# Kernel tuning notes

Measured on AMD Instinct MI355X. Metric: run time of the kernel, lower is better.

## Reference

```python
import jax, jax.numpy as jnp
import numpy as np

D_MODEL = 256
N_HEADS = 8
D_HEAD = D_MODEL // N_HEADS
SCALE = D_HEAD ** -0.5
LN_EPS = 1e-5


def _layernorm(x, gamma, beta):
    mu = jnp.mean(x, axis=-1, keepdims=True)
    var = jnp.mean(jnp.square(x - mu), axis=-1, keepdims=True)
    return (x - mu) * jax.lax.rsqrt(var + LN_EPS) * gamma + beta


def setup_inputs() -> dict:
    key = jax.random.key(0)
    ks = jax.random.split(key, 8)
    B, N_q, N_kv = 2, 1024, 8192
    q = jax.random.normal(ks[0], (B, N_q, D_MODEL), dtype=jnp.float32)
    kv = jax.random.normal(ks[1], (B, N_kv, D_MODEL), dtype=jnp.float32)
    attn_bias = jax.random.normal(ks[2], (B, N_HEADS, N_q, N_kv), dtype=jnp.float32)
    s = D_MODEL ** -0.5
    Wq = jax.random.normal(ks[3], (D_MODEL, D_MODEL), dtype=jnp.float32) * s
    Wk = jax.random.normal(ks[4], (D_MODEL, D_MODEL), dtype=jnp.float32) * s
    Wv = jax.random.normal(ks[5], (D_MODEL, D_MODEL), dtype=jnp.float32) * s
    Wo = jax.random.normal(ks[6], (D_MODEL, D_MODEL), dtype=jnp.float32) * s
    gamma_q = jnp.ones((D_MODEL,), jnp.float32)
    beta_q = jnp.zeros((D_MODEL,), jnp.float32)
    gamma_kv = jnp.ones((D_MODEL,), jnp.float32)
    beta_kv = jnp.zeros((D_MODEL,), jnp.float32)
    return dict(q=q, kv=kv, attn_bias=attn_bias, Wq=Wq, Wk=Wk, Wv=Wv, Wo=Wo,
                gamma_q=gamma_q, beta_q=beta_q, gamma_kv=gamma_kv, beta_kv=beta_kv)


def reference(q, kv, attn_bias, Wq, Wk, Wv, Wo, gamma_q, beta_q, gamma_kv, beta_kv):
    B, N_q, D = q.shape
    N_kv = kv.shape[1]
    q_n = _layernorm(q, gamma_q, beta_q)
    kv_n = _layernorm(kv, gamma_kv, beta_kv)
    # nn.Linear(x) = x @ W.T ; reshape to (B, H, N, dh)
    Q = (q_n @ Wq.T).reshape(B, N_q, N_HEADS, D_HEAD).transpose(0, 2, 1, 3)
    K = (kv_n @ Wk.T).reshape(B, N_kv, N_HEADS, D_HEAD).transpose(0, 2, 1, 3)
    V = (kv_n @ Wv.T).reshape(B, N_kv, N_HEADS, D_HEAD).transpose(0, 2, 1, 3)
    scores = jnp.einsum('bhqd,bhkd->bhqk', Q, K) * SCALE + attn_bias
    attn = jax.nn.softmax(scores, axis=-1)
    out = jnp.einsum('bhqk,bhkd->bhqd', attn, V)
    out = out.transpose(0, 2, 1, 3).reshape(B, N_q, D)
    return q + out @ Wo.T
```

## Files before the change

### kernel.cpp

```cpp
#include <hip/hip_runtime.h>
#include <hip/hip_bf16.h>
#include <stdint.h>

#define H 8
#define NQ 1024
#define NKV 8192
#define DM 256
#define DH 32
#define KVBLK 128
#define KSPLIT 8
#define NITER (NKV / KSPLIT / KVBLK)
#define SCALE 0.17677669529663687f

typedef __attribute__((ext_vector_type(8))) __bf16 bf16x8;
typedef __attribute__((ext_vector_type(4))) float f32x4;

__device__ inline unsigned short f2bf(float f) {
  unsigned int u = __builtin_bit_cast(unsigned int, f);
  u = (u + 0x7FFFu + ((u >> 16) & 1u)) >> 16;
  return (unsigned short)u;
}

__global__ void prep_kernel(const float* __restrict__ q, const float* __restrict__ kv,
                            const float* __restrict__ gq, const float* __restrict__ bq,
                            const float* __restrict__ gkv, const float* __restrict__ bkv,
                            const float* __restrict__ Wq, const float* __restrict__ Wk,
                            const float* __restrict__ Wv, const float* __restrict__ Wo,
                            unsigned short* __restrict__ qn, unsigned short* __restrict__ kvn,
                            unsigned short* __restrict__ Wqb, unsigned short* __restrict__ Wkb,
                            unsigned short* __restrict__ Wvb, unsigned short* __restrict__ Wob) {
  int bx = blockIdx.x;
  if (bx < 256) {
    int widx = bx >> 6, blk = bx & 63;
    const float* src; unsigned short* dst;
    if (widx == 0)      { src = Wq; dst = Wqb; }
    else if (widx == 1) { src = Wk; dst = Wkb; }
    else if (widx == 2) { src = Wv; dst = Wvb; }
    else                { src = Wo; dst = Wob; }
    int i = (blk * 256 + threadIdx.x) * 4;
    float4 v = *(const float4*)(src + i);
    unsigned int lo = (unsigned int)f2bf(v.x) | ((unsigned int)f2bf(v.y) << 16);
    unsigned int hi = (unsigned int)f2bf(v.z) | ((unsigned int)f2bf(v.w) << 16);
    *(uint2*)(dst + i) = make_uint2(lo, hi);
    return;
  }
  int row = (bx - 256) * 64 + (threadIdx.x >> 2);
  int l4 = threadIdx.x & 3;
  const float* src; const float* ga; const float* be; unsigned short* dst;
  if (row < 2048) {
    src = q + (long)row * DM; ga = gq; be = bq; dst = qn + (long)row * DM;
  } else {
    int r2 = row - 2048;
    src = kv + (long)r2 * DM; ga = gkv; be = bkv; dst = kvn + (long)r2 * DM;
  }
  int c0 = l4 * 64;
  float s = 0.f, ss = 0.f;
  float4 xv[16];
#pragma unroll
  for (int i = 0; i < 16; i++) {
    float4 v = *(const float4*)(src + c0 + i * 4);
    xv[i] = v;
    s += v.x + v.y + v.z + v.w;
    ss += v.x * v.x + v.y * v.y + v.z * v.z + v.w * v.w;
  }
  s += __shfl_xor(s, 1, 4);  s += __shfl_xor(s, 2, 4);
  ss += __shfl_xor(ss, 1, 4); ss += __shfl_xor(ss, 2, 4);
  float mean = s * (1.0f / 256.0f);
  float var = ss * (1.0f / 256.0f) - mean * mean;
  float rs = 1.0f / sqrtf(var + 1e-5f);
#pragma unroll
  for (int i = 0; i < 8; i++) {
    float4 a = xv[2 * i], b = xv[2 * i + 1];
    float4 g0 = *(const float4*)(ga + c0 + i * 8);
    float4 g1 = *(const float4*)(ga + c0 + i * 8 + 4);
    float4 b0 = *(const float4*)(be + c0 + i * 8);
    float4 b1 = *(const float4*)(be + c0 + i * 8 + 4);
    unsigned short t[8];
    t[0] = f2bf((a.x - mean) * rs * g0.x + b0.x);
    t[1] = f2bf((a.y - mean) * rs * g0.y + b0.y);
    t[2] = f2bf((a.z - mean) * rs * g0.z + b0.z);
    t[3] = f2bf((a.w - mean) * rs * g0.w + b0.w);
    t[4] = f2bf((b.x - mean) * rs * g1.x + b1.x);
    t[5] = f2bf((b.y - mean) * rs * g1.y + b1.y);
    t[6] = f2bf((b.z - mean) * rs * g1.z + b1.z);
    t[7] = f2bf((b.w - mean) * rs * g1.w + b1.w);
    unsigned int u0 = (unsigned int)t[0] | ((unsigned int)t[1] << 16);
    unsigned int u1 = (unsigned int)t[2] | ((unsigned int)t[3] << 16);
    unsigned int u2 = (unsigned int)t[4] | ((unsigned int)t[5] << 16);
    unsigned int u3 = (unsigned int)t[6] | ((unsigned int)t[7] << 16);
    *(uint4*)(dst + c0 + i * 8) = make_uint4(u0, u1, u2, u3);
  }
}

__global__ void proj_all_kernel(const unsigned short* __restrict__ qn, const unsigned short* __restrict__ kvn,
                                const unsigned short* __restrict__ Wqb, const unsigned short* __restrict__ Wkb,
                                const unsigned short* __restrict__ Wvb,
                                unsigned short* __restrict__ Qw, unsigned short* __restrict__ Kw,
                                unsigned short* __restrict__ Vtw) {
  int bx = blockIdx.x;
  const unsigned short* X; const unsigned short* Wb; unsigned short* out;
  int Nper, mode, mb;
  if (bx < 32)       { X = qn;  Wb = Wqb; out = Qw;  Nper = NQ;  mode = 0; mb = bx; }
  else if (bx < 288) { X = kvn; Wb = Wkb; out = Kw;  Nper = NKV; mode = 0; mb = bx - 32; }
  else               { X = kvn; Wb = Wvb; out = Vtw; Nper = NKV; mode = 1; mb = bx - 288; }

  int w = threadIdx.x >> 6, lane = threadIdx.x & 63;
  int c = lane & 15, g = lane >> 4;
  int mbase = mb * 64 + w * 16;
  f32x4 acc[16];
#pragma unroll
  for (int i = 0; i < 16; i++) acc[i] = (f32x4){0.f, 0.f, 0.f, 0.f};
  const unsigned short* arow = X + (long)(mbase + c) * DM + g * 8;
#pragma unroll
  for (int ks = 0; ks < 8; ks++) {
    bf16x8 af = *(const bf16x8*)(arow + ks * 32);
#pragma unroll
    for (int nt = 0; nt < 16; nt++) {
      bf16x8 bf = *(const bf16x8*)(Wb + (long)(nt * 16 + c) * DM + ks * 32 + g * 8);
      acc[nt] = __builtin_amdgcn_mfma_f32_16x16x32_bf16(af, bf, acc[nt], 0, 0, 0);
    }
  }
#pragma unroll
  for (int nt = 0; nt < 16; nt++) {
#pragma unroll
    for (int r = 0; r < 4; r++) {
      int m = mbase + 4 * g + r;
      int n = nt * 16 + c;
      int b = (m >= Nper) ? 1 : 0;
      int i = m - b * Nper;
      int h = n >> 5, dd = n & 31;
      long idx;
      if (mode == 0) idx = ((long)(b * H + h) * Nper + i) * DH + dd;
      else           idx = ((long)(b * H + h) * DH + dd) * (long)Nper + i;
      out[idx] = f2bf(acc[nt][r]);
    }
  }
}

__global__ __launch_bounds__(256, 4) void attn_kernel(
    const unsigned short* __restrict__ Qw, const unsigned short* __restrict__ Kw,
    const unsigned short* __restrict__ Vtw, const float* __restrict__ bias,
    float* __restrict__ Opart, float* __restrict__ Mpart, float* __restrict__ Lpart) {
  __shared__ __align__(16) unsigned short Klds[KVBLK * 40];
  __shared__ __align__(16) unsigned short Vlds[DH * 136];
  __shared__ __align__(16) unsigned short Plds[4][16 * 136];

  int bx = blockIdx.x;
  int s = bx & 7, qt = (bx >> 3) & 15, bh = bx >> 7;
  int tid = threadIdx.x;
  int w = tid >> 6, lane = tid & 63, c = lane & 15, g = lane >> 4;

  const f32x4 fzero = {0.f, 0.f, 0.f, 0.f};

  bf16x8 qfrag = *(const bf16x8*)(Qw + ((long)(bh * NQ + qt * 64 + w * 16 + c)) * DH + g * 8);

  const float* brow = bias + ((long)bh * NQ + qt * 64 + w * 16 + c) * (long)NKV + 4 * g;

  const unsigned short* Kbase = Kw + ((long)bh * NKV) * DH;
  const unsigned short* Vbase = Vtw + ((long)bh * DH) * NKV;

  float m_run = -1e30f;
  float l_run = 0.f;
  f32x4 oacc[2] = {fzero, fzero};

#pragma unroll 1
  for (int it = 0; it < NITER; it++) {
    int k0 = (it * KSPLIT + s) * KVBLK;

    f32x4 bfrag[8];
#pragma unroll
    for (int t = 0; t < 8; t++)
      bfrag[t] = *(const f32x4*)(brow + k0 + t * 16);

    {
      const unsigned short* src = Kbase + (long)k0 * DH;
#pragma unroll
      for (int rp = 0; rp < 2; rp++) {
        int row = (tid >> 2) + rp * 64;
        int q4 = tid & 3;
        *(uint4*)(&Klds[row * 40 + q4 * 8]) = *(const uint4*)(src + row * DH + q4 * 8);
      }
#pragma unroll
      for (int rp = 0; rp < 2; rp++) {
        int u = tid + rp * 256;
        int d = u >> 4, q16 = u & 15;
        *(uint4*)(&Vlds[d * 136 + q16 * 8]) = *(const uint4*)(Vbase + (long)d * NKV + k0 + q16 * 8);
      }
    }
    __syncthreads();

    f32x4 sacc[8];
#pragma unroll
    for (int t = 0; t < 8; t++) {
      bf16x8 kf = *(const bf16x8*)(&Klds[(t * 16 + c) * 40 + g * 8]);
      sacc[t] = __builtin_amdgcn_mfma_f32_16x16x32_bf16(kf, qfrag, fzero, 0, 0, 0);
    }
#pragma unroll
    for (int t = 0; t < 8; t++) {
#pragma unroll
      for (int r = 0; r < 4; r++)
        sacc[t][r] = fmaf(sacc[t][r], SCALE, bfrag[t][r]);
    }

    float v = -1e30f;
#pragma unroll
    for (int t = 0; t < 8; t++)
      v = fmaxf(v, fmaxf(fmaxf(sacc[t][0], sacc[t][1]), fmaxf(sacc[t][2], sacc[t][3])));
    v = fmaxf(v, __shfl_xor(v, 16));
    v = fmaxf(v, __shfl_xor(v, 32));
    float mnew = fmaxf(m_run, v);
    float al = __expf(m_run - mnew);
    m_run = mnew;
    float rsum = 0.f;
#pragma unroll
    for (int t = 0; t < 8; t++) {
      float p0 = __expf(sacc[t][0] - mnew);
      float p1 = __expf(sacc[t][1] - mnew);
      float p2 = __expf(sacc[t][2] - mnew);
      float p3 = __expf(sacc[t][3] - mnew);
      rsum += (p0 + p1) + (p2 + p3);
      uint2 pk;
      pk.x = (unsigned int)f2bf(p0) | ((unsigned int)f2bf(p1) << 16);
      pk.y = (unsigned int)f2bf(p2) | ((unsigned int)f2bf(p3) << 16);
      *(uint2*)(&Plds[w][c * 136 + t * 16 + 4 * g]) = pk;
    }
    rsum += __shfl_xor(rsum, 16);
    rsum += __shfl_xor(rsum, 32);
    l_run = l_run * al + rsum;

    float alq[4];
#pragma unroll
    for (int r = 0; r < 4; r++) alq[r] = __shfl(al, 4 * g + r);
#pragma unroll
    for (int r = 0; r < 4; r++) { oacc[0][r] *= alq[r]; oacc[1][r] *= alq[r]; }

#pragma unroll
    for (int ch = 0; ch < 4; ch++) {
      bf16x8 pf = *(const bf16x8*)(&Plds[w][c * 136 + ch * 32 + g * 8]);
#pragma unroll
      for (int dt = 0; dt < 2; dt++) {
        bf16x8 vf = *(const bf16x8*)(&Vlds[(dt * 16 + c) * 136 + ch * 32 + g * 8]);
        oacc[dt] = __builtin_amdgcn_mfma_f32_16x16x32_bf16(pf, vf, oacc[dt], 0, 0, 0);
      }
    }
    __syncthreads();
  }
  float* Op = Opart + (long)bx * (64 * 32);
#pragma unroll
  for (int dt = 0; dt < 2; dt++)
#pragma unroll
    for (int r = 0; r < 4; r++)
      Op[(w * 16 + 4 * g + r) * 32 + dt * 16 + c] = oacc[dt][r];
  if (g == 0) {
    Mpart[(long)bx * 64 + w * 16 + c] = m_run;
    Lpart[(long)bx * 64 + w * 16 + c] = l_run;
  }
}

__global__ void merge_outproj_kernel(const float* __restrict__ Opart, const float* __restrict__ Mpart,
                                     const float* __restrict__ Lpart, const unsigned short* __restrict__ Wob,
                                     const float* __restrict__ qin, float* __restrict__ out) {
  __shared__ __align__(16) unsigned short OmT[16][264];

  int bx = blockIdx.x;
  int b = bx >> 6, qt = (bx >> 2) & 15, q4 = bx & 3;
  int tid = threadIdx.x;

  int row16 = tid >> 4;
  int d0 = (tid & 15) * 2;
  int rowA = q4 * 16 + row16;
#pragma unroll 1
  for (int h = 0; h < 8; h++) {
    long pbase = ((long)(b * 8 + h) * 16 + qt) * 8;
    float mg = -1e30f, ms[8];
#pragma unroll
    for (int si = 0; si < 8; si++) {
      ms[si] = Mpart[(pbase + si) * 64 + rowA];
      mg = fmaxf(mg, ms[si]);
    }
    float Lg = 0.f;
    float o0 = 0.f, o1 = 0.f;
#pragma unroll
    for (int si = 0; si < 8; si++) {
      float wsc = __expf(ms[si] - mg);
      Lg += Lpart[(pbase + si) * 64 + rowA] * wsc;
      const float* op = Opart + (pbase + si) * 2048 + rowA * 32 + d0;
      o0 += op[0] * wsc;
      o1 += op[1] * wsc;
    }
    float inv = 1.0f / Lg;
    unsigned int u = (unsigned int)f2bf(o0 * inv) | ((unsigned int)f2bf(o1 * inv) << 16);
    *(unsigned int*)(&OmT[row16][h * 32 + d0]) = u;
  }
  __syncthreads();

  int w = tid >> 6, lane = tid & 63;
  int c = lane & 15, g = lane >> 4;
  long mglob = (long)b * NQ + qt * 64 + q4 * 16;
  f32x4 acc[4];
#pragma unroll
  for (int i = 0; i < 4; i++) acc[i] = (f32x4){0.f, 0.f, 0.f, 0.f};
#pragma unroll
  for (int ks = 0; ks < 8; ks++) {
    bf16x8 af = *(const bf16x8*)(&OmT[c][ks * 32 + g * 8]);
#pragma unroll
    for (int j = 0; j < 4; j++) {
      int nt = w * 4 + j;
      bf16x8 bf = *(const bf16x8*)(Wob + (long)(nt * 16 + c) * DM + ks * 32 + g * 8);
      acc[j] = __builtin_amdgcn_mfma_f32_16x16x32_bf16(af, bf, acc[j], 0, 0, 0);
    }
  }
#pragma unroll
  for (int j = 0; j < 4; j++) {
#pragma unroll
    for (int r = 0; r < 4; r++) {
      long m = mglob + 4 * g + r;
      int n = (w * 4 + j) * 16 + c;
      out[m * DM + n] = qin[m * DM + n] + acc[j][r];
    }
  }
}

extern "C" void kernel_launch(void* const* d_in, const int* in_sizes, int n_in,
                              void* d_out, int out_size, void* d_ws, size_t ws_size,
                              hipStream_t stream) {
  (void)in_sizes; (void)n_in; (void)out_size; (void)ws_size;
  const float* q    = (const float*)d_in[0];
  const float* kv   = (const float*)d_in[1];
  const float* bias = (const float*)d_in[2];
  const float* Wq   = (const float*)d_in[3];
  const float* Wk   = (const float*)d_in[4];
  const float* Wv   = (const float*)d_in[5];
  const float* Wo   = (const float*)d_in[6];
  const float* gq   = (const float*)d_in[7];
  const float* bq   = (const float*)d_in[8];
  const float* gkv  = (const float*)d_in[9];
  const float* bkv  = (const float*)d_in[10];
  float* out = (float*)d_out;

  char* ws = (char*)d_ws;
  size_t off = 0;
  auto alloc = [&](size_t bytes) -> void* {
    void* p = ws + off;
    off += (bytes + 255) & ~(size_t)255;
    return p;
  };
  unsigned short* Wqb  = (unsigned short*)alloc(65536 * 2);
  unsigned short* Wkb  = (unsigned short*)alloc(65536 * 2);
  unsigned short* Wvb  = (unsigned short*)alloc(65536 * 2);
  unsigned short* Wob  = (unsigned short*)alloc(65536 * 2);
  unsigned short* qn   = (unsigned short*)alloc((size_t)2048 * 256 * 2);
  unsigned short* kvn  = (unsigned short*)alloc((size_t)16384 * 256 * 2);
  unsigned short* Qw   = (unsigned short*)alloc((size_t)2048 * 256 * 2);
  unsigned short* Kw   = (unsigned short*)alloc((size_t)16384 * 256 * 2);
  unsigned short* Vtw  = (unsigned short*)alloc((size_t)16384 * 256 * 2);
  float* Opart = (float*)alloc((size_t)2048 * 2048 * 4);
  float* Mpart = (float*)alloc((size_t)2048 * 64 * 4);
  float* Lpart = (float*)alloc((size_t)2048 * 64 * 4);

  prep_kernel<<<544, 256, 0, stream>>>(q, kv, gq, bq, gkv, bkv, Wq, Wk, Wv, Wo,
                                       qn, kvn, Wqb, Wkb, Wvb, Wob);

  proj_all_kernel<<<544, 256, 0, stream>>>(qn, kvn, Wqb, Wkb, Wvb, Qw, Kw, Vtw);

  attn_kernel<<<2048, 256, 0, stream>>>(Qw, Kw, Vtw, bias, Opart, Mpart, Lpart);

  merge_outproj_kernel<<<128, 256, 0, stream>>>(Opart, Mpart, Lpart, Wob, q, out);
}
```

Before: 222.7 us.

## Fuse layernorm into projection GEMM and register-prefetch K/V and bias in attention

Splits weight conversion into its own small kernel and folds the layernorm of q/kv directly into the projection kernel. Normalized bf16 activations are now built in registers instead of going through a global round trip. The attention loop is restructured to prefetch the next K/V tile and the next bias fragments into registers while the current tile is computed. This hides global load latency at the cost of more registers and extra barriers. kv rows are now read and normalized twice, once each for the K and V projections.

```diff
diff --git a/kernel.cpp b/kernel.cpp
--- a/kernel.cpp
+++ b/kernel.cpp
@@ -21,99 +21,82 @@
   return (unsigned short)u;
 }
 
-__global__ void prep_kernel(const float* __restrict__ q, const float* __restrict__ kv,
-                            const float* __restrict__ gq, const float* __restrict__ bq,
-                            const float* __restrict__ gkv, const float* __restrict__ bkv,
-                            const float* __restrict__ Wq, const float* __restrict__ Wk,
-                            const float* __restrict__ Wv, const float* __restrict__ Wo,
-                            unsigned short* __restrict__ qn, unsigned short* __restrict__ kvn,
-                            unsigned short* __restrict__ Wqb, unsigned short* __restrict__ Wkb,
-                            unsigned short* __restrict__ Wvb, unsigned short* __restrict__ Wob) {
-  int bx = blockIdx.x;
-  if (bx < 256) {
-    int widx = bx >> 6, blk = bx & 63;
-    const float* src; unsigned short* dst;
-    if (widx == 0)      { src = Wq; dst = Wqb; }
-    else if (widx == 1) { src = Wk; dst = Wkb; }
-    else if (widx == 2) { src = Wv; dst = Wvb; }
-    else                { src = Wo; dst = Wob; }
-    int i = (blk * 256 + threadIdx.x) * 4;
-    float4 v = *(const float4*)(src + i);
+__global__ void wconv_kernel(const float* __restrict__ Wq, const float* __restrict__ Wk,
+                             const float* __restrict__ Wv, const float* __restrict__ Wo,
+                             unsigned short* __restrict__ Wqb, unsigned short* __restrict__ Wkb,
+                             unsigned short* __restrict__ Wvb, unsigned short* __restrict__ Wob) {
+  long i = ((long)blockIdx.x * 256 + threadIdx.x) * 16;
+  int widx = (int)(i >> 16);
+  int off = (int)(i & 65535);
+  const float* src; unsigned short* dst;
+  if (widx == 0)      { src = Wq; dst = Wqb; }
+  else if (widx == 1) { src = Wk; dst = Wkb; }
+  else if (widx == 2) { src = Wv; dst = Wvb; }
+  else                { src = Wo; dst = Wob; }
+#pragma unroll
+  for (int j = 0; j < 4; j++) {
+    float4 v = *(const float4*)(src + off + j * 4);
     unsigned int lo = (unsigned int)f2bf(v.x) | ((unsigned int)f2bf(v.y) << 16);
     unsigned int hi = (unsigned int)f2bf(v.z) | ((unsigned int)f2bf(v.w) << 16);
-    *(uint2*)(dst + i) = make_uint2(lo, hi);
-    return;
-  }
-  int row = (bx - 256) * 64 + (threadIdx.x >> 2);
-  int l4 = threadIdx.x & 3;
-  const float* src; const float* ga; const float* be; unsigned short* dst;
-  if (row < 2048) {
-    src = q + (long)row * DM; ga = gq; be = bq; dst = qn + (long)row * DM;
-  } else {
-    int r2 = row - 2048;
-    src = kv + (long)r2 * DM; ga = gkv; be = bkv; dst = kvn + (long)r2 * DM;
-  }
-  int c0 = l4 * 64;
+    *(uint2*)(dst + off + j * 4) = make_uint2(lo, hi);
+  }
+}
+
+__global__ void ln_proj_kernel(const float* __restrict__ qin, const float* __restrict__ kvin,
+                               const float* __restrict__ gq, const float* __restrict__ bq,
+                               const float* __restrict__ gkv, const float* __restrict__ bkv,
+                               const unsigned short* __restrict__ Wqb, const unsigned short* __restrict__ Wkb,
+                               const unsigned short* __restrict__ Wvb,
+                               unsigned short* __restrict__ Qw, unsigned short* __restrict__ Kw,
+                               unsigned short* __restrict__ Vtw) {
+  int bx = blockIdx.x;
+  const float* X; const float* ga; const float* be;
+  const unsigned short* Wb; unsigned short* out;
+  int Nper, mode, mb;
+  if (bx < 32)       { X = qin;  ga = gq;  be = bq;  Wb = Wqb; out = Qw;  Nper = NQ;  mode = 0; mb = bx; }
+  else if (bx < 288) { X = kvin; ga = gkv; be = bkv; Wb = Wkb; out = Kw;  Nper = NKV; mode = 0; mb = bx - 32; }
+  else               { X = kvin; ga = gkv; be = bkv; Wb = Wvb; out = Vtw; Nper = NKV; mode = 1; mb = bx - 288; }
+
+  int w = threadIdx.x >> 6, lane = threadIdx.x & 63;
+  int c = lane & 15, g = lane >> 4;
+  int mbase = mb * 64 + w * 16;
+  const float* xp = X + (long)(mbase + c) * DM + g * 8;
+
   float s = 0.f, ss = 0.f;
-  float4 xv[16];
-#pragma unroll
-  for (int i = 0; i < 16; i++) {
-    float4 v = *(const float4*)(src + c0 + i * 4);
-    xv[i] = v;
-    s += v.x + v.y + v.z + v.w;
-    ss += v.x * v.x + v.y * v.y + v.z * v.z + v.w * v.w;
-  }
-  s += __shfl_xor(s, 1, 4);  s += __shfl_xor(s, 2, 4);
-  ss += __shfl_xor(ss, 1, 4); ss += __shfl_xor(ss, 2, 4);
+#pragma unroll
+  for (int ks = 0; ks < 8; ks++) {
+    float4 a = *(const float4*)(xp + ks * 32);
+    float4 b = *(const float4*)(xp + ks * 32 + 4);
+    s += (a.x + a.y) + (a.z + a.w) + (b.x + b.y) + (b.z + b.w);
+    ss += (a.x * a.x + a.y * a.y) + (a.z * a.z + a.w * a.w)
+        + (b.x * b.x + b.y * b.y) + (b.z * b.z + b.w * b.w);
+  }
+  s += __shfl_xor(s, 16);  s += __shfl_xor(s, 32);
+  ss += __shfl_xor(ss, 16); ss += __shfl_xor(ss, 32);
   float mean = s * (1.0f / 256.0f);
   float var = ss * (1.0f / 256.0f) - mean * mean;
   float rs = 1.0f / sqrtf(var + 1e-5f);
-#pragma unroll
-  for (int i = 0; i < 8; i++) {
-    float4 a = xv[2 * i], b = xv[2 * i + 1];
-    float4 g0 = *(const float4*)(ga + c0 + i * 8);
-    float4 g1 = *(const float4*)(ga + c0 + i * 8 + 4);
-    float4 b0 = *(const float4*)(be + c0 + i * 8);
-    float4 b1 = *(const float4*)(be + c0 + i * 8 + 4);
-    unsigned short t[8];
-    t[0] = f2bf((a.x - mean) * rs * g0.x + b0.x);
-    t[1] = f2bf((a.y - mean) * rs * g0.y + b0.y);
-    t[2] = f2bf((a.z - mean) * rs * g0.z + b0.z);
-    t[3] = f2bf((a.w - mean) * rs * g0.w + b0.w);
-    t[4] = f2bf((b.x - mean) * rs * g1.x + b1.x);
-    t[5] = f2bf((b.y - mean) * rs * g1.y + b1.y);
-    t[6] = f2bf((b.z - mean) * rs * g1.z + b1.z);
-    t[7] = f2bf((b.w - mean) * rs * g1.w + b1.w);
-    unsigned int u0 = (unsigned int)t[0] | ((unsigned int)t[1] << 16);
-    unsigned int u1 = (unsigned int)t[2] | ((unsigned int)t[3] << 16);
-    unsigned int u2 = (unsigned int)t[4] | ((unsigned int)t[5] << 16);
-    unsigned int u3 = (unsigned int)t[6] | ((unsigned int)t[7] << 16);
-    *(uint4*)(dst + c0 + i * 8) = make_uint4(u0, u1, u2, u3);
-  }
-}
-
-__global__ void proj_all_kernel(const unsigned short* __restrict__ qn, const unsigned short* __restrict__ kvn,
-                                const unsigned short* __restrict__ Wqb, const unsigned short* __restrict__ Wkb,
-                                const unsigned short* __restrict__ Wvb,
-                                unsigned short* __restrict__ Qw, unsigned short* __restrict__ Kw,
-                                unsigned short* __restrict__ Vtw) {
-  int bx = blockIdx.x;
-  const unsigned short* X; const unsigned short* Wb; unsigned short* out;
-  int Nper, mode, mb;
-  if (bx < 32)       { X = qn;  Wb = Wqb; out = Qw;  Nper = NQ;  mode = 0; mb = bx; }
-  else if (bx < 288) { X = kvn; Wb = Wkb; out = Kw;  Nper = NKV; mode = 0; mb = bx - 32; }
-  else               { X = kvn; Wb = Wvb; out = Vtw; Nper = NKV; mode = 1; mb = bx - 288; }
-
-  int w = threadIdx.x >> 6, lane = threadIdx.x & 63;
-  int c = lane & 15, g = lane >> 4;
-  int mbase = mb * 64 + w * 16;
+
   f32x4 acc[16];
 #pragma unroll
   for (int i = 0; i < 16; i++) acc[i] = (f32x4){0.f, 0.f, 0.f, 0.f};
-  const unsigned short* arow = X + (long)(mbase + c) * DM + g * 8;
 #pragma unroll
   for (int ks = 0; ks < 8; ks++) {
-    bf16x8 af = *(const bf16x8*)(arow + ks * 32);
+    float4 a = *(const float4*)(xp + ks * 32);
+    float4 b = *(const float4*)(xp + ks * 32 + 4);
+    float4 g0 = *(const float4*)(ga + ks * 32 + g * 8);
+    float4 g1 = *(const float4*)(ga + ks * 32 + g * 8 + 4);
+    float4 b0 = *(const float4*)(be + ks * 32 + g * 8);
+    float4 b1 = *(const float4*)(be + ks * 32 + g * 8 + 4);
+    unsigned int u0 = (unsigned int)f2bf((a.x - mean) * rs * g0.x + b0.x)
+                    | ((unsigned int)f2bf((a.y - mean) * rs * g0.y + b0.y) << 16);
+    unsigned int u1 = (unsigned int)f2bf((a.z - mean) * rs * g0.z + b0.z)
+                    | ((unsigned int)f2bf((a.w - mean) * rs * g0.w + b0.w) << 16);
+    unsigned int u2 = (unsigned int)f2bf((b.x - mean) * rs * g1.x + b1.x)
+                    | ((unsigned int)f2bf((b.y - mean) * rs * g1.y + b1.y) << 16);
+    unsigned int u3 = (unsigned int)f2bf((b.z - mean) * rs * g1.z + b1.z)
+                    | ((unsigned int)f2bf((b.w - mean) * rs * g1.w + b1.w) << 16);
+    bf16x8 af = __builtin_bit_cast(bf16x8, make_uint4(u0, u1, u2, u3));
 #pragma unroll
     for (int nt = 0; nt < 16; nt++) {
       bf16x8 bf = *(const bf16x8*)(Wb + (long)(nt * 16 + c) * DM + ks * 32 + g * 8);
@@ -159,36 +142,42 @@
   const unsigned short* Kbase = Kw + ((long)bh * NKV) * DH;
   const unsigned short* Vbase = Vtw + ((long)bh * DH) * NKV;
 
+  int krow = tid >> 2, kq4 = tid & 3;
+  int vd0 = tid >> 4, vq16 = tid & 15;
+
+  uint4 kA[2], vA[2], kB[2], vB[2];
+  f32x4 bfrag[8];
+
+  auto k0_of = [&](int it) { return (it * KSPLIT + s) * KVBLK; };
+  auto issue_kv = [&](int it, uint4* kr, uint4* vr) {
+    int k0 = k0_of(it);
+#pragma unroll
+    for (int rp = 0; rp < 2; rp++)
+      kr[rp] = *(const uint4*)(Kbase + (long)(k0 + krow + rp * 64) * DH + kq4 * 8);
+#pragma unroll
+    for (int rp = 0; rp < 2; rp++)
+      vr[rp] = *(const uint4*)(Vbase + (long)(vd0 + rp * 16) * NKV + k0 + vq16 * 8);
+  };
+  auto write_kv = [&](const uint4* kr, const uint4* vr) {
+#pragma unroll
+    for (int rp = 0; rp < 2; rp++)
+      *(uint4*)(&Klds[(krow + rp * 64) * 40 + kq4 * 8]) = kr[rp];
+#pragma unroll
+    for (int rp = 0; rp < 2; rp++)
+      *(uint4*)(&Vlds[(vd0 + rp * 16) * 136 + vq16 * 8]) = vr[rp];
+  };
+  auto issue_bias = [&](int it) {
+    int k0 = k0_of(it);
+#pragma unroll
+    for (int t = 0; t < 8; t++)
+      bfrag[t] = *(const f32x4*)(brow + k0 + t * 16);
+  };
+
   float m_run = -1e30f;
   float l_run = 0.f;
   f32x4 oacc[2] = {fzero, fzero};
 
-#pragma unroll 1
-  for (int it = 0; it < NITER; it++) {
-    int k0 = (it * KSPLIT + s) * KVBLK;
-
-    f32x4 bfrag[8];
-#pragma unroll
-    for (int t = 0; t < 8; t++)
-      bfrag[t] = *(const f32x4*)(brow + k0 + t * 16);
-
-    {
-      const unsigned short* src = Kbase + (long)k0 * DH;
-#pragma unroll
-      for (int rp = 0; rp < 2; rp++) {
-        int row = (tid >> 2) + rp * 64;
-        int q4 = tid & 3;
-        *(uint4*)(&Klds[row * 40 + q4 * 8]) = *(const uint4*)(src + row * DH + q4 * 8);
-      }
-#pragma unroll
-      for (int rp = 0; rp < 2; rp++) {
-        int u = tid + rp * 256;
-        int d = u >> 4, q16 = u & 15;
-        *(uint4*)(&Vlds[d * 136 + q16 * 8]) = *(const uint4*)(Vbase + (long)d * NKV + k0 + q16 * 8);
-      }
-    }
-    __syncthreads();
-
+  auto compute_iter = [&](int nextIt) {
     f32x4 sacc[8];
 #pragma unroll
     for (int t = 0; t < 8; t++) {
@@ -201,6 +190,7 @@
       for (int r = 0; r < 4; r++)
         sacc[t][r] = fmaf(sacc[t][r], SCALE, bfrag[t][r]);
     }
+    if (nextIt < NITER) issue_bias(nextIt);
 
     float v = -1e30f;
 #pragma unroll
@@ -243,8 +233,26 @@
         oacc[dt] = __builtin_amdgcn_mfma_f32_16x16x32_bf16(pf, vf, oacc[dt], 0, 0, 0);
       }
     }
+  };
+
+  issue_kv(0, kA, vA);
+  issue_bias(0);
+
+#pragma unroll 1
+  for (int it2 = 0; it2 < NITER; it2 += 2) {
     __syncthreads();
-  }
+    write_kv(kA, vA);
+    __syncthreads();
+    if (it2 + 1 < NITER) issue_kv(it2 + 1, kB, vB);
+    compute_iter(it2 + 1);
+
+    __syncthreads();
+    write_kv(kB, vB);
+    __syncthreads();
+    if (it2 + 2 < NITER) issue_kv(it2 + 2, kA, vA);
+    compute_iter(it2 + 2);
+  }
+
   float* Op = Opart + (long)bx * (64 * 32);
 #pragma unroll
   for (int dt = 0; dt < 2; dt++)
@@ -349,8 +357,6 @@
   unsigned short* Wkb  = (unsigned short*)alloc(65536 * 2);
   unsigned short* Wvb  = (unsigned short*)alloc(65536 * 2);
   unsigned short* Wob  = (unsigned short*)alloc(65536 * 2);
-  unsigned short* qn   = (unsigned short*)alloc((size_t)2048 * 256 * 2);
-  unsigned short* kvn  = (unsigned short*)alloc((size_t)16384 * 256 * 2);
   unsigned short* Qw   = (unsigned short*)alloc((size_t)2048 * 256 * 2);
   unsigned short* Kw   = (unsigned short*)alloc((size_t)16384 * 256 * 2);
   unsigned short* Vtw  = (unsigned short*)alloc((size_t)16384 * 256 * 2);
@@ -358,10 +364,10 @@
   float* Mpart = (float*)alloc((size_t)2048 * 64 * 4);
   float* Lpart = (float*)alloc((size_t)2048 * 64 * 4);
 
-  prep_kernel<<<544, 256, 0, stream>>>(q, kv, gq, bq, gkv, bkv, Wq, Wk, Wv, Wo,
-                                       qn, kvn, Wqb, Wkb, Wvb, Wob);
-
-  proj_all_kernel<<<544, 256, 0, stream>>>(qn, kvn, Wqb, Wkb, Wvb, Qw, Kw, Vtw);
+  wconv_kernel<<<64, 256, 0, stream>>>(Wq, Wk, Wv, Wo, Wqb, Wkb, Wvb, Wob);
+
+  ln_proj_kernel<<<544, 256, 0, stream>>>(q, kv, gq, bq, gkv, bkv,
+                                          Wqb, Wkb, Wvb, Qw, Kw, Vtw);
 
   attn_kernel<<<2048, 256, 0, stream>>>(Qw, Kw, Vtw, bias, Opart, Mpart, Lpart);
 
```

Result: slower. 297.2 us (+33.5%).
